# Kernel optimization log

Measured on AMD Instinct MI355X. Metric: run time of the kernel, lower is better.

The kernel has to match this reference:

```python
import jax, jax.numpy as jnp
import numpy as np

H = 1024
V = 50000
E_SOUND, E_NUM = 40, 5
D_SOUND, D_NUM = 32, 32
IN_DIM = H + D_SOUND + D_NUM  # GRU input size
B, L = 128, 128


def setup_inputs() -> dict:
    key = jax.random.key(0)
    ks = jax.random.split(key, 16)
    s = lambda k, shape: jax.random.normal(k, shape, jnp.float32) * 0.02
    return {
        "input_seq": jax.random.randint(ks[0], (B,), 0, V),
        "last_hidden": jax.random.normal(ks[1], (1, B, H), jnp.float32),
        "encoder_outputs": jax.random.normal(ks[2], (L, B, H), jnp.float32),
        "char2num": jax.random.randint(ks[3], (V,), 0, E_NUM),
        "char2final": jax.random.randint(ks[4], (V,), 0, E_SOUND),
        "emb": s(ks[5], (V, H)),
        "sound_emb": s(ks[6], (E_SOUND, D_SOUND)),
        "num_emb": s(ks[7], (E_NUM, D_NUM)),
        "W_ih": s(ks[8], (3 * H, IN_DIM)),
        "W_hh": s(ks[9], (3 * H, H)),
        "b_ih": jnp.zeros((3 * H,), jnp.float32),
        "b_hh": jnp.zeros((3 * H,), jnp.float32),
        "W_attn": s(ks[10], (H, H)),
        "b_attn": jnp.zeros((H,), jnp.float32),
        "W_cat": s(ks[11], (H, 2 * H)),
        "b_cat": jnp.zeros((H,), jnp.float32),
        "W_out": s(ks[12], (V, H)),
        "b_out": jnp.zeros((V,), jnp.float32),
    }


def _gru_cell(x, h, W_ih, W_hh, b_ih, b_hh):
    # PyTorch GRU gate order: r, z, n
    gi = x @ W_ih.T + b_ih
    gh = h @ W_hh.T + b_hh
    i_r, i_z, i_n = jnp.split(gi, 3, axis=-1)
    h_r, h_z, h_n = jnp.split(gh, 3, axis=-1)
    r = jax.nn.sigmoid(i_r + h_r)
    z = jax.nn.sigmoid(i_z + h_z)
    n = jnp.tanh(i_n + r * h_n)
    return (1.0 - z) * n + z * h


def reference(input_seq, last_hidden, encoder_outputs, char2num, char2final,
              emb, sound_emb, num_emb, W_ih, W_hh, b_ih, b_hh,
              W_attn, b_attn, W_cat, b_cat, W_out, b_out):
    # Embeddings (eval mode -> dropout is identity)
    e = emb[input_seq]                             # [B,H]
    num_ids = char2num[input_seq]                  # [B]
    snd_ids = char2final[input_seq]                # [B]
    x = jnp.concatenate([e, sound_emb[snd_ids], num_emb[num_ids]], -1)  # [B,IN_DIM]

    # Single-step single-layer GRU
    h_new = _gru_cell(x, last_hidden[0], W_ih, W_hh, b_ih, b_hh)  # [B,H]
    hidden = h_new[None]                            # [1,B,H]
    rnn_output = h_new                              # [B,H]

    # Luong 'general' attention, batched (replaces the nested-loop .mm calls)
    proj = jnp.einsum('lbh,kh->lbk', encoder_outputs, W_attn) + b_attn  # [L,B,H]
    energies = jnp.einsum('bh,lbh->bl', rnn_output, proj)               # [B,L]
    attn_weights = jax.nn.softmax(energies, axis=1)[:, None, :]         # [B,1,L]
    context = jnp.einsum('bl,lbh->bh', attn_weights[:, 0], encoder_outputs)

    concat_out = jnp.tanh(jnp.concatenate([rnn_output, context], -1) @ W_cat.T + b_cat)
    output = concat_out @ W_out.T + b_out           # [B,V]
    return output, hidden, attn_weights
```

## Files before the change

### kernel.cpp

```cpp
#include <hip/hip_runtime.h>
#include <hip/hip_bf16.h>
#include <cstddef>

#define B_   128
#define L_   128
#define H_   1024
#define V_   50000
#define INDIM 1088

typedef short short8 __attribute__((ext_vector_type(8)));
typedef unsigned short ushort8 __attribute__((ext_vector_type(8)));
typedef unsigned short ushort4v __attribute__((ext_vector_type(4)));
typedef float f32x4 __attribute__((ext_vector_type(4)));

static __device__ __forceinline__ unsigned short f2bf(float f) {
    unsigned u = __builtin_bit_cast(unsigned, f);
    u = u + 0x7FFFu + ((u >> 16) & 1u);
    return (unsigned short)(u >> 16);
}
static __device__ __forceinline__ float bf2f(unsigned short h) {
    unsigned u = ((unsigned)h) << 16;
    return __builtin_bit_cast(float, u);
}
static __device__ __forceinline__ float sigm(float v) {
    return 1.f / (1.f + __expf(-v));
}

__global__ __launch_bounds__(256) void prep_kernel(
    const int* __restrict__ seq, const int* __restrict__ c2n,
    const int* __restrict__ c2f, const float* __restrict__ emb,
    const float* __restrict__ semb, const float* __restrict__ nemb,
    const float* __restrict__ lh,
    unsigned short* __restrict__ x_hi, unsigned short* __restrict__ x_lo,
    unsigned short* __restrict__ h_hi, unsigned short* __restrict__ h_lo)
{
    const int b = blockIdx.x, t = threadIdx.x;
    const int idx = seq[b];
    for (int i = t; i < 528; i += 256) {
        float4 v;
        unsigned short *dh, *dl;
        int off;
        if (i < 272) {
            if (i < 256) {
                v = *(const float4*)&emb[(size_t)idx * H_ + i * 4];
            } else {
                const int j = i - 256;
                if (j < 8) v = *(const float4*)&semb[c2f[idx] * 32 + j * 4];
                else       v = *(const float4*)&nemb[c2n[idx] * 32 + (j - 8) * 4];
            }
            dh = x_hi + (size_t)b * INDIM; dl = x_lo + (size_t)b * INDIM; off = i * 4;
        } else {
            const int j = i - 272;
            v = *(const float4*)&lh[(size_t)b * H_ + j * 4];
            dh = h_hi + (size_t)b * H_; dl = h_lo + (size_t)b * H_; off = j * 4;
        }
        const float fv[4] = {v.x, v.y, v.z, v.w};
        ushort4v hh, ll;
#pragma unroll
        for (int e = 0; e < 4; e++) {
            hh[e] = f2bf(fv[e]);
            ll[e] = f2bf(fv[e] - bf2f(hh[e]));
        }
        *(ushort4v*)&dh[off] = hh;
        *(ushort4v*)&dl[off] = ll;
    }
}

template<bool WT, bool SPLIT, bool TANH>
static __device__ __forceinline__ void sgemm_body(
    const unsigned short* __restrict__ Ah, const unsigned short* __restrict__ Al, int lda,
    const float* __restrict__ W, int ldw,
    const float* __restrict__ bias,
    float* __restrict__ C, int ldc, size_t pstride,
    int N, int k_len0, int k_lenB)
{
    extern __shared__ char smem_raw[];
    typedef unsigned short RowT[72];
    RowT* As_h = (RowT*)(smem_raw);
    RowT* Ws_h = (RowT*)(smem_raw + 18432);
    RowT* As_l = (RowT*)(smem_raw + 27648);
    RowT* Ws_l = (RowT*)(smem_raw + 46080);

    const int t    = threadIdx.x;
    const int lane = t & 63;
    const int wv   = t >> 6;
    const int wr   = wv >> 1;
    const int wc   = wv & 1;
    const int n0   = blockIdx.x * 64;
    const int l15  = lane & 15;
    const int g    = lane >> 4;

    const int y     = blockIdx.y;
    const int k_off = (y == 0) ? 0 : k_len0 + (y - 1) * k_lenB;
    const int k_len = (y == 0) ? k_len0 : k_lenB;
    float* Cp = C + (size_t)y * pstride;

    const int ar = t >> 3;
    const int ac = (t & 7) * 8;
    const int wn = t >> 2, wq = t & 3;
    const int nk = t >> 4, nn4 = (t & 15) * 4;

    f32x4 acc[4][2];
#pragma unroll
    for (int i = 0; i < 4; i++)
#pragma unroll
        for (int j = 0; j < 2; j++) acc[i][j] = (f32x4){0.f, 0.f, 0.f, 0.f};

#define LOAD_A(K0, RA, RAL) do {                                               \
    _Pragma("unroll")                                                          \
    for (int i_ = 0; i_ < 4; i_++)                                             \
        RA[i_] = *(const ushort8*)&Ah[(size_t)(ar + i_ * 32) * lda + (K0) + ac]; \
    if constexpr (SPLIT) {                                                     \
        _Pragma("unroll")                                                      \
        for (int i_ = 0; i_ < 4; i_++)                                         \
            RAL[i_] = *(const ushort8*)&Al[(size_t)(ar + i_ * 32) * lda + (K0) + ac]; \
    }                                                                          \
} while (0)

#define LOAD_W(K0, RW) do {                                                    \
    if constexpr (WT) {                                                        \
        const bool ok_ = (n0 + wn) < N;                                        \
        const float* wb_ = W + (size_t)(n0 + wn) * ldw + (K0);                 \
        _Pragma("unroll")                                                      \
        for (int j_ = 0; j_ < 4; j_++)                                         \
            RW[j_] = ok_ ? *(const float4*)&wb_[j_ * 16 + wq * 4]              \
                         : make_float4(0.f, 0.f, 0.f, 0.f);                    \
    } else {                                                                   \
        _Pragma("unroll")                                                      \
        for (int j_ = 0; j_ < 4; j_++)                                         \
            RW[j_] = *(const float4*)&W[(size_t)((K0) + nk + j_ * 16) * ldw + n0 + nn4]; \
    }                                                                          \
} while (0)

#define STAGE_REGS(RA, RAL, RW) do {                                           \
    _Pragma("unroll")                                                          \
    for (int i_ = 0; i_ < 4; i_++) {                                           \
        *(ushort8*)&As_h[ar + i_ * 32][ac] = RA[i_];                           \
        if constexpr (SPLIT) *(ushort8*)&As_l[ar + i_ * 32][ac] = RAL[i_];     \
    }                                                                          \
    if constexpr (WT) {                                                        \
        _Pragma("unroll")                                                      \
        for (int j_ = 0; j_ < 4; j_++) {                                       \
            const float fv_[4] = {RW[j_].x, RW[j_].y, RW[j_].z, RW[j_].w};     \
            ushort4v hh_, ll_;                                                 \
            _Pragma("unroll")                                                  \
            for (int e_ = 0; e_ < 4; e_++) {                                   \
                hh_[e_] = f2bf(fv_[e_]);                                       \
                if constexpr (SPLIT) ll_[e_] = f2bf(fv_[e_] - bf2f(hh_[e_]));  \
            }                                                                  \
            *(ushort4v*)&Ws_h[wn][j_ * 16 + wq * 4] = hh_;                     \
            if constexpr (SPLIT) *(ushort4v*)&Ws_l[wn][j_ * 16 + wq * 4] = ll_; \
        }                                                                      \
    } else {                                                                   \
        _Pragma("unroll")                                                      \
        for (int j_ = 0; j_ < 4; j_++) {                                       \
            const float fv_[4] = {RW[j_].x, RW[j_].y, RW[j_].z, RW[j_].w};     \
            _Pragma("unroll")                                                  \
            for (int e_ = 0; e_ < 4; e_++) {                                   \
                const unsigned short hb_ = f2bf(fv_[e_]);                      \
                Ws_h[nn4 + e_][nk + j_ * 16] = hb_;                            \
                if constexpr (SPLIT)                                           \
                    Ws_l[nn4 + e_][nk + j_ * 16] = f2bf(fv_[e_] - bf2f(hb_));  \
            }                                                                  \
        }                                                                      \
    }                                                                          \
} while (0)

    const int k_end = k_off + k_len;

    ushort8 ra[4], ral[4], nra[4], nral[4];
    float4 rw0[4], rw1[4], rw2[4];

    LOAD_A(k_off, ra, ral);
    LOAD_W(k_off, rw0);
    if constexpr (!SPLIT) {
        if (k_off + 64 < k_end) LOAD_W(k_off + 64, rw1);
    }

    for (int k0 = k_off; k0 < k_end; k0 += 64) {
        const bool m1 = (k0 + 64) < k_end;
        const bool m2 = (k0 + 128) < k_end;
        if (m1) {
            LOAD_A(k0 + 64, nra, nral);
            if constexpr (SPLIT) LOAD_W(k0 + 64, rw1);
        }

        STAGE_REGS(ra, ral, rw0);
        __syncthreads();

        if constexpr (!SPLIT) {
            if (m2) LOAD_W(k0 + 128, rw2);
        }

#pragma unroll
        for (int ks = 0; ks < 2; ks++) {
            const int ko = ks * 32 + g * 8;
            short8 ah[4], bh[2];
#pragma unroll
            for (int mi = 0; mi < 4; mi++)
                ah[mi] = *(const short8*)&As_h[wr * 64 + mi * 16 + l15][ko];
#pragma unroll
            for (int ni = 0; ni < 2; ni++)
                bh[ni] = *(const short8*)&Ws_h[wc * 32 + ni * 16 + l15][ko];
            if constexpr (SPLIT) {
                short8 al[4], bl[2];
#pragma unroll
                for (int mi = 0; mi < 4; mi++)
                    al[mi] = *(const short8*)&As_l[wr * 64 + mi * 16 + l15][ko];
#pragma unroll
                for (int ni = 0; ni < 2; ni++)
                    bl[ni] = *(const short8*)&Ws_l[wc * 32 + ni * 16 + l15][ko];
#pragma unroll
                for (int mi = 0; mi < 4; mi++)
#pragma unroll
                    for (int ni = 0; ni < 2; ni++) {
                        acc[mi][ni] = __builtin_amdgcn_mfma_f32_16x16x32_bf16(ah[mi], bh[ni], acc[mi][ni], 0, 0, 0);
                        acc[mi][ni] = __builtin_amdgcn_mfma_f32_16x16x32_bf16(ah[mi], bl[ni], acc[mi][ni], 0, 0, 0);
                        acc[mi][ni] = __builtin_amdgcn_mfma_f32_16x16x32_bf16(al[mi], bh[ni], acc[mi][ni], 0, 0, 0);
                    }
            } else {
#pragma unroll
                for (int mi = 0; mi < 4; mi++)
#pragma unroll
                    for (int ni = 0; ni < 2; ni++)
                        acc[mi][ni] = __builtin_amdgcn_mfma_f32_16x16x32_bf16(ah[mi], bh[ni], acc[mi][ni], 0, 0, 0);
            }
        }
        __syncthreads();

        if (m1) {
#pragma unroll
            for (int i = 0; i < 4; i++) {
                ra[i] = nra[i];
                if constexpr (SPLIT) ral[i] = nral[i];
            }
#pragma unroll
            for (int j = 0; j < 4; j++) {
                rw0[j] = rw1[j];
                if constexpr (!SPLIT) rw1[j] = rw2[j];
            }
        }
    }
#undef LOAD_A
#undef LOAD_W
#undef STAGE_REGS

#pragma unroll
    for (int mi = 0; mi < 4; mi++) {
#pragma unroll
        for (int ni = 0; ni < 2; ni++) {
            const int col = n0 + wc * 32 + ni * 16 + l15;
            if (col < N) {
                const float bb = bias ? bias[col] : 0.f;
#pragma unroll
                for (int r = 0; r < 4; r++) {
                    const int row = wr * 64 + mi * 16 + g * 4 + r;
                    float v = acc[mi][ni][r] + bb;
                    if (TANH) v = tanhf(v);
                    Cp[(size_t)row * ldc + col] = v;
                }
            }
        }
    }
}

template<bool WT, bool SPLIT, bool TANH>
__global__ __launch_bounds__(256, 2) void sgemm(
    const unsigned short* __restrict__ Ah, const unsigned short* __restrict__ Al, int lda,
    const float* __restrict__ W, int ldw,
    const float* __restrict__ bias,
    float* __restrict__ C, int ldc, size_t pstride,
    int N, int k_len0, int k_lenB)
{
    sgemm_body<WT, SPLIT, TANH>(Ah, Al, lda, W, ldw, bias, C, ldc, pstride, N, k_len0, k_lenB);
}

__global__ __launch_bounds__(256, 2) void gru_gemm(
    const unsigned short* __restrict__ x_hi, const unsigned short* __restrict__ x_lo,
    const float* __restrict__ W_ih,
    const unsigned short* __restrict__ h_hi, const unsigned short* __restrict__ h_lo,
    const float* __restrict__ W_hh,
    float* __restrict__ gi, float* __restrict__ gh)
{
    if (blockIdx.z == 0)
        sgemm_body<true, true, false>(x_hi, x_lo, INDIM, W_ih, INDIM, nullptr,
                                      gi, 3072, (size_t)128 * 3072, 3072, 320, 256);
    else
        sgemm_body<true, true, false>(h_hi, h_lo, H_, W_hh, H_, nullptr,
                                      gh, 3072, (size_t)128 * 3072, 3072, 256, 256);
}

__global__ __launch_bounds__(256) void gru_gates_kernel(
    const float* __restrict__ gi, const float* __restrict__ gh,
    const float* __restrict__ b_ih, const float* __restrict__ b_hh,
    const float* __restrict__ h_prev,
    float* __restrict__ hid_out,
    unsigned short* __restrict__ cat_hi, unsigned short* __restrict__ cat_lo)
{
    const int id = blockIdx.x * 256 + threadIdx.x;
    const int b = id >> 10, j = id & 1023;
    const size_t base = (size_t)b * 3072 + j;
    float ir = b_ih[j], iz = b_ih[1024 + j], in_ = b_ih[2048 + j];
    float hr = b_hh[j], hz = b_hh[1024 + j], hn = b_hh[2048 + j];
#pragma unroll
    for (int p = 0; p < 4; p++) {
        const float* gp = gi + (size_t)p * (128 * 3072);
        const float* hp = gh + (size_t)p * (128 * 3072);
        ir += gp[base]; iz += gp[base + 1024]; in_ += gp[base + 2048];
        hr += hp[base]; hz += hp[base + 1024]; hn += hp[base + 2048];
    }
    const float r = sigm(ir + hr);
    const float z = sigm(iz + hz);
    const float n = tanhf(in_ + r * hn);
    const float h = (1.f - z) * n + z * h_prev[id];
    hid_out[id] = h;
    const unsigned short hb = f2bf(h);
    cat_hi[(size_t)b * 2048 + j] = hb;
    cat_lo[(size_t)b * 2048 + j] = f2bf(h - bf2f(hb));
}

__global__ __launch_bounds__(512) void energy_partial_kernel(
    const float* __restrict__ qp, const float* __restrict__ enc,
    float* __restrict__ epart)
{
    const int s = blockIdx.x, b = blockIdx.y;
    const int t = threadIdx.x, lane = t & 63, wv = t >> 6;
    __shared__ float q_s[256];
    if (t < 256) {
        const size_t o = (size_t)b * H_ + s * 256 + t;
        q_s[t] = qp[o] + qp[o + 131072] + qp[o + 262144] + qp[o + 393216];
    }
    __syncthreads();
    const float4 qv = *(const float4*)&q_s[lane * 4];
    const float* encb = enc + (size_t)b * H_ + s * 256;
    for (int l0 = 0; l0 < 16; l0++) {
        const int l = wv * 16 + l0;
        float4 ev = *(const float4*)&encb[(size_t)l * (B_ * H_) + lane * 4];
        float p = ev.x * qv.x + ev.y * qv.y + ev.z * qv.z + ev.w * qv.w;
#pragma unroll
        for (int off = 32; off > 0; off >>= 1) p += __shfl_xor(p, off);
        if (lane == 0) epart[((size_t)b * 128 + l) * 4 + s] = p;
    }
}

__global__ __launch_bounds__(256) void context_softmax_kernel(
    const float* __restrict__ epart, const float* __restrict__ enc,
    unsigned short* __restrict__ cat_hi, float* __restrict__ attnw)
{
    const int s = blockIdx.x, b = blockIdx.y, t = threadIdx.x;
    const int lane = t & 63, wv = t >> 6;
    __shared__ float w_s[128];
    __shared__ float red[4];

    float e = -INFINITY;
    if (t < 128) {
        float4 pe = *(const float4*)&epart[((size_t)b * 128 + t) * 4];
        e = pe.x + pe.y + pe.z + pe.w;
    }
    float mx = e;
#pragma unroll
    for (int off = 32; off > 0; off >>= 1) mx = fmaxf(mx, __shfl_xor(mx, off));
    if (lane == 0) red[wv] = mx;
    __syncthreads();
    const float gm = fmaxf(fmaxf(red[0], red[1]), fmaxf(red[2], red[3]));
    __syncthreads();
    float ex = (t < 128) ? __expf(e - gm) : 0.f;
    float sm = ex;
#pragma unroll
    for (int off = 32; off > 0; off >>= 1) sm += __shfl_xor(sm, off);
    if (lane == 0) red[wv] = sm;
    __syncthreads();
    const float gs = red[0] + red[1] + red[2] + red[3];
    if (t < 128) {
        const float w = ex / gs;
        w_s[t] = w;
        if (s == 0) attnw[(size_t)b * L_ + t] = w;
    }
    __syncthreads();

    const int h = s * 256 + t;
    const float* encb = enc + (size_t)b * H_ + h;
    float c = 0.f;
#pragma unroll 4
    for (int l = 0; l < 128; l++)
        c += w_s[l] * encb[(size_t)l * (B_ * H_)];
    cat_hi[(size_t)b * 2048 + 1024 + h] = f2bf(c);
}

__global__ __launch_bounds__(256) void co_reduce_kernel(
    const float* __restrict__ co_part, const float* __restrict__ b_cat,
    unsigned short* __restrict__ co_hi)
{
    const int id = blockIdx.x * 256 + threadIdx.x;
    const int j = id & 1023;
    float s = b_cat[j];
#pragma unroll
    for (int p = 0; p < 4; p++) s += co_part[(size_t)p * 131072 + id];
    co_hi[id] = f2bf(tanhf(s));
}

extern "C" void kernel_launch(void* const* d_in, const int* in_sizes, int n_in,
                              void* d_out, int out_size, void* d_ws, size_t ws_size,
                              hipStream_t stream)
{
    const int*   seq    = (const int*)  d_in[0];
    const float* lh     = (const float*)d_in[1];
    const float* enc    = (const float*)d_in[2];
    const int*   c2n    = (const int*)  d_in[3];
    const int*   c2f    = (const int*)  d_in[4];
    const float* emb    = (const float*)d_in[5];
    const float* semb   = (const float*)d_in[6];
    const float* nemb   = (const float*)d_in[7];
    const float* W_ih   = (const float*)d_in[8];
    const float* W_hh   = (const float*)d_in[9];
    const float* b_ih   = (const float*)d_in[10];
    const float* b_hh   = (const float*)d_in[11];
    const float* W_attn = (const float*)d_in[12];
    const float* W_cat  = (const float*)d_in[14];
    const float* b_cat  = (const float*)d_in[15];
    const float* W_out  = (const float*)d_in[16];
    const float* b_out  = (const float*)d_in[17];

    float* out    = (float*)d_out;
    float* hidden = out + (size_t)B_ * V_;
    float* attnw  = hidden + (size_t)B_ * H_;

    unsigned short* x_hi   = (unsigned short*)d_ws;
    unsigned short* x_lo   = x_hi   + (size_t)128 * INDIM;
    unsigned short* h_hi   = x_lo   + (size_t)128 * INDIM;
    unsigned short* h_lo   = h_hi   + (size_t)128 * 1024;
    unsigned short* cat_hi = h_lo   + (size_t)128 * 1024;
    unsigned short* cat_lo = cat_hi + (size_t)128 * 2048;
    unsigned short* co_hi  = cat_lo + (size_t)128 * 2048;
    float* fbase   = (float*)(co_hi + (size_t)128 * 1024);
    float* gi_part = fbase;
    float* gh_part = gi_part + (size_t)4 * 128 * 3072;
    float* q_part  = fbase;
    float* co_part = q_part + (size_t)4 * 128 * 1024;
    float* epart   = co_part + (size_t)4 * 128 * 1024;

    const int SMEM_SPLIT = 55296;
    const int SMEM_PLAIN = 27648;

    hipLaunchKernelGGL(prep_kernel, dim3(B_), dim3(256), 0, stream,
                       seq, c2n, c2f, emb, semb, nemb, lh, x_hi, x_lo, h_hi, h_lo);
    hipLaunchKernelGGL(gru_gemm, dim3(48, 4, 2), dim3(256), SMEM_SPLIT, stream,
                       x_hi, x_lo, W_ih, h_hi, h_lo, W_hh, gi_part, gh_part);
    hipLaunchKernelGGL(gru_gates_kernel, dim3(512), dim3(256), 0, stream,
                       gi_part, gh_part, b_ih, b_hh, lh, hidden, cat_hi, cat_lo);
    hipLaunchKernelGGL((sgemm<false, true, false>), dim3(16, 4), dim3(256), SMEM_SPLIT, stream,
                       cat_hi, cat_lo, 2048, W_attn, H_, (const float*)nullptr,
                       q_part, H_, (size_t)128 * 1024, H_, 256, 256);
    hipLaunchKernelGGL(energy_partial_kernel, dim3(4, 128), dim3(512), 0, stream,
                       q_part, enc, epart);
    hipLaunchKernelGGL(context_softmax_kernel, dim3(4, 128), dim3(256), 0, stream,
                       epart, enc, cat_hi, attnw);
    hipLaunchKernelGGL((sgemm<true, false, false>), dim3(16, 4), dim3(256), SMEM_PLAIN, stream,
                       cat_hi, cat_hi, 2048, W_cat, 2048, (const float*)nullptr,
                       co_part, H_, (size_t)128 * 1024, H_, 512, 512);
    hipLaunchKernelGGL(co_reduce_kernel, dim3(512), dim3(256), 0, stream,
                       co_part, b_cat, co_hi);
    hipLaunchKernelGGL((sgemm<true, false, false>), dim3((V_ + 63) / 64, 1), dim3(256), SMEM_PLAIN, stream,
                       co_hi, co_hi, H_, W_out, H_, b_out,
                       out, V_, (size_t)0, V_, H_, H_);
}
```

Measured before the change: 160.3 us.

## Replace LDS-tiled GEMMs with per-wave register GEMMs reading weights directly

Replaces the shared-memory tiled sgemm with wave-level GEMMs. Each wave owns 16 output columns across all 128 batch rows, loads its weight slice straight from global memory, converts it with packed bf16 conversion instructions, and feeds MFMA with A fragments read directly from global/L2. W_attn is pre-transposed and split into bf16 hi/lo inside the prep kernel so the attention-projection GEMM can read contiguous rows. This removes LDS staging and barriers and lets the weight stream flow without a block tile, but the A operand is reloaded from cache by every wave without LDS reuse. The hidden-state-independent transpose of W_attn is now redone on every call as extra work.

After: 302.8 us. 88.9% more time.

```diff
diff --git a/kernel.cpp b/kernel.cpp
--- a/kernel.cpp
+++ b/kernel.cpp
@@ -9,7 +9,6 @@
 #define INDIM 1088
 
 typedef short short8 __attribute__((ext_vector_type(8)));
-typedef unsigned short ushort8 __attribute__((ext_vector_type(8)));
 typedef unsigned short ushort4v __attribute__((ext_vector_type(4)));
 typedef float f32x4 __attribute__((ext_vector_type(4)));
 
@@ -26,268 +25,268 @@
     return 1.f / (1.f + __expf(-v));
 }
 
+static __device__ __forceinline__ unsigned cvt_pk(float lo, float hi) {
+    unsigned r;
+    asm("v_cvt_pk_bf16_f32 %0, %1, %2" : "=v"(r) : "v"(lo), "v"(hi));
+    return r;
+}
+static __device__ __forceinline__ short8 cvt8(float4 a, float4 b) {
+    union { unsigned u[4]; short8 s; } r;
+    r.u[0] = cvt_pk(a.x, a.y); r.u[1] = cvt_pk(a.z, a.w);
+    r.u[2] = cvt_pk(b.x, b.y); r.u[3] = cvt_pk(b.z, b.w);
+    return r.s;
+}
+static __device__ __forceinline__ void cvt8_split(float4 a, float4 b, short8& hi, short8& lo) {
+    const float f[8] = {a.x, a.y, a.z, a.w, b.x, b.y, b.z, b.w};
+    union { unsigned u[4]; short8 s; } rh, rl;
+#pragma unroll
+    for (int i = 0; i < 4; i++) {
+        const unsigned p = cvt_pk(f[2 * i], f[2 * i + 1]);
+        const float r0 = __builtin_bit_cast(float, p << 16);
+        const float r1 = __builtin_bit_cast(float, p & 0xFFFF0000u);
+        rh.u[i] = p;
+        rl.u[i] = cvt_pk(f[2 * i] - r0, f[2 * i + 1] - r1);
+    }
+    hi = rh.s; lo = rl.s;
+}
+
+#define MFMA(a, b, c) __builtin_amdgcn_mfma_f32_16x16x32_bf16((a), (b), (c), 0, 0, 0)
+
 __global__ __launch_bounds__(256) void prep_kernel(
     const int* __restrict__ seq, const int* __restrict__ c2n,
     const int* __restrict__ c2f, const float* __restrict__ emb,
     const float* __restrict__ semb, const float* __restrict__ nemb,
-    const float* __restrict__ lh,
+    const float* __restrict__ lh, const float* __restrict__ W_attn,
     unsigned short* __restrict__ x_hi, unsigned short* __restrict__ x_lo,
-    unsigned short* __restrict__ h_hi, unsigned short* __restrict__ h_lo)
-{
-    const int b = blockIdx.x, t = threadIdx.x;
-    const int idx = seq[b];
-    for (int i = t; i < 528; i += 256) {
-        float4 v;
-        unsigned short *dh, *dl;
-        int off;
-        if (i < 272) {
-            if (i < 256) {
-                v = *(const float4*)&emb[(size_t)idx * H_ + i * 4];
+    unsigned short* __restrict__ h_hi, unsigned short* __restrict__ h_lo,
+    unsigned short* __restrict__ wt_hi, unsigned short* __restrict__ wt_lo)
+{
+    __shared__ float tile[64][65];
+    const int t = threadIdx.x;
+    if (blockIdx.x < 128) {
+        const int b = blockIdx.x;
+        const int idx = seq[b];
+        for (int i = t; i < 528; i += 256) {
+            float4 v;
+            unsigned short *dh, *dl;
+            int off;
+            if (i < 272) {
+                if (i < 256) {
+                    v = *(const float4*)&emb[(size_t)idx * H_ + i * 4];
+                } else {
+                    const int j = i - 256;
+                    if (j < 8) v = *(const float4*)&semb[c2f[idx] * 32 + j * 4];
+                    else       v = *(const float4*)&nemb[c2n[idx] * 32 + (j - 8) * 4];
+                }
+                dh = x_hi + (size_t)b * INDIM; dl = x_lo + (size_t)b * INDIM; off = i * 4;
             } else {
-                const int j = i - 256;
-                if (j < 8) v = *(const float4*)&semb[c2f[idx] * 32 + j * 4];
-                else       v = *(const float4*)&nemb[c2n[idx] * 32 + (j - 8) * 4];
-            }
-            dh = x_hi + (size_t)b * INDIM; dl = x_lo + (size_t)b * INDIM; off = i * 4;
-        } else {
-            const int j = i - 272;
-            v = *(const float4*)&lh[(size_t)b * H_ + j * 4];
-            dh = h_hi + (size_t)b * H_; dl = h_lo + (size_t)b * H_; off = j * 4;
-        }
-        const float fv[4] = {v.x, v.y, v.z, v.w};
-        ushort4v hh, ll;
-#pragma unroll
-        for (int e = 0; e < 4; e++) {
-            hh[e] = f2bf(fv[e]);
-            ll[e] = f2bf(fv[e] - bf2f(hh[e]));
-        }
-        *(ushort4v*)&dh[off] = hh;
-        *(ushort4v*)&dl[off] = ll;
-    }
-}
-
-template<bool WT, bool SPLIT, bool TANH>
-static __device__ __forceinline__ void sgemm_body(
-    const unsigned short* __restrict__ Ah, const unsigned short* __restrict__ Al, int lda,
-    const float* __restrict__ W, int ldw,
-    const float* __restrict__ bias,
-    float* __restrict__ C, int ldc, size_t pstride,
-    int N, int k_len0, int k_lenB)
-{
-    extern __shared__ char smem_raw[];
-    typedef unsigned short RowT[72];
-    RowT* As_h = (RowT*)(smem_raw);
-    RowT* Ws_h = (RowT*)(smem_raw + 18432);
-    RowT* As_l = (RowT*)(smem_raw + 27648);
-    RowT* Ws_l = (RowT*)(smem_raw + 46080);
-
-    const int t    = threadIdx.x;
-    const int lane = t & 63;
-    const int wv   = t >> 6;
-    const int wr   = wv >> 1;
-    const int wc   = wv & 1;
-    const int n0   = blockIdx.x * 64;
-    const int l15  = lane & 15;
-    const int g    = lane >> 4;
-
-    const int y     = blockIdx.y;
-    const int k_off = (y == 0) ? 0 : k_len0 + (y - 1) * k_lenB;
-    const int k_len = (y == 0) ? k_len0 : k_lenB;
-    float* Cp = C + (size_t)y * pstride;
-
-    const int ar = t >> 3;
-    const int ac = (t & 7) * 8;
-    const int wn = t >> 2, wq = t & 3;
-    const int nk = t >> 4, nn4 = (t & 15) * 4;
-
-    f32x4 acc[4][2];
-#pragma unroll
-    for (int i = 0; i < 4; i++)
-#pragma unroll
-        for (int j = 0; j < 2; j++) acc[i][j] = (f32x4){0.f, 0.f, 0.f, 0.f};
-
-#define LOAD_A(K0, RA, RAL) do {                                               \
-    _Pragma("unroll")                                                          \
-    for (int i_ = 0; i_ < 4; i_++)                                             \
-        RA[i_] = *(const ushort8*)&Ah[(size_t)(ar + i_ * 32) * lda + (K0) + ac]; \
-    if constexpr (SPLIT) {                                                     \
-        _Pragma("unroll")                                                      \
-        for (int i_ = 0; i_ < 4; i_++)                                         \
-            RAL[i_] = *(const ushort8*)&Al[(size_t)(ar + i_ * 32) * lda + (K0) + ac]; \
-    }                                                                          \
-} while (0)
-
-#define LOAD_W(K0, RW) do {                                                    \
-    if constexpr (WT) {                                                        \
-        const bool ok_ = (n0 + wn) < N;                                        \
-        const float* wb_ = W + (size_t)(n0 + wn) * ldw + (K0);                 \
-        _Pragma("unroll")                                                      \
-        for (int j_ = 0; j_ < 4; j_++)                                         \
-            RW[j_] = ok_ ? *(const float4*)&wb_[j_ * 16 + wq * 4]              \
-                         : make_float4(0.f, 0.f, 0.f, 0.f);                    \
-    } else {                                                                   \
-        _Pragma("unroll")                                                      \
-        for (int j_ = 0; j_ < 4; j_++)                                         \
-            RW[j_] = *(const float4*)&W[(size_t)((K0) + nk + j_ * 16) * ldw + n0 + nn4]; \
-    }                                                                          \
-} while (0)
-
-#define STAGE_REGS(RA, RAL, RW) do {                                           \
-    _Pragma("unroll")                                                          \
-    for (int i_ = 0; i_ < 4; i_++) {                                           \
-        *(ushort8*)&As_h[ar + i_ * 32][ac] = RA[i_];                           \
-        if constexpr (SPLIT) *(ushort8*)&As_l[ar + i_ * 32][ac] = RAL[i_];     \
-    }                                                                          \
-    if constexpr (WT) {                                                        \
-        _Pragma("unroll")                                                      \
-        for (int j_ = 0; j_ < 4; j_++) {                                       \
-            const float fv_[4] = {RW[j_].x, RW[j_].y, RW[j_].z, RW[j_].w};     \
-            ushort4v hh_, ll_;                                                 \
-            _Pragma("unroll")                                                  \
-            for (int e_ = 0; e_ < 4; e_++) {                                   \
-                hh_[e_] = f2bf(fv_[e_]);                                       \
-                if constexpr (SPLIT) ll_[e_] = f2bf(fv_[e_] - bf2f(hh_[e_]));  \
-            }                                                                  \
-            *(ushort4v*)&Ws_h[wn][j_ * 16 + wq * 4] = hh_;                     \
-            if constexpr (SPLIT) *(ushort4v*)&Ws_l[wn][j_ * 16 + wq * 4] = ll_; \
-        }                                                                      \
-    } else {                                                                   \
-        _Pragma("unroll")                                                      \
-        for (int j_ = 0; j_ < 4; j_++) {                                       \
-            const float fv_[4] = {RW[j_].x, RW[j_].y, RW[j_].z, RW[j_].w};     \
-            _Pragma("unroll")                                                  \
-            for (int e_ = 0; e_ < 4; e_++) {                                   \
-                const unsigned short hb_ = f2bf(fv_[e_]);                      \
-                Ws_h[nn4 + e_][nk + j_ * 16] = hb_;                            \
-                if constexpr (SPLIT)                                           \
-                    Ws_l[nn4 + e_][nk + j_ * 16] = f2bf(fv_[e_] - bf2f(hb_));  \
-            }                                                                  \
-        }                                                                      \
-    }                                                                          \
-} while (0)
-
-    const int k_end = k_off + k_len;
-
-    ushort8 ra[4], ral[4], nra[4], nral[4];
-    float4 rw0[4], rw1[4], rw2[4];
-
-    LOAD_A(k_off, ra, ral);
-    LOAD_W(k_off, rw0);
-    if constexpr (!SPLIT) {
-        if (k_off + 64 < k_end) LOAD_W(k_off + 64, rw1);
-    }
-
-    for (int k0 = k_off; k0 < k_end; k0 += 64) {
-        const bool m1 = (k0 + 64) < k_end;
-        const bool m2 = (k0 + 128) < k_end;
-        if (m1) {
-            LOAD_A(k0 + 64, nra, nral);
-            if constexpr (SPLIT) LOAD_W(k0 + 64, rw1);
-        }
-
-        STAGE_REGS(ra, ral, rw0);
+                const int j = i - 272;
+                v = *(const float4*)&lh[(size_t)b * H_ + j * 4];
+                dh = h_hi + (size_t)b * H_; dl = h_lo + (size_t)b * H_; off = j * 4;
+            }
+            const float fv[4] = {v.x, v.y, v.z, v.w};
+            ushort4v hh, ll;
+#pragma unroll
+            for (int e = 0; e < 4; e++) {
+                hh[e] = f2bf(fv[e]);
+                ll[e] = f2bf(fv[e] - bf2f(hh[e]));
+            }
+            *(ushort4v*)&dh[off] = hh;
+            *(ushort4v*)&dl[off] = ll;
+        }
+    } else {
+        const int bid = blockIdx.x - 128;
+        const int n0 = (bid & 15) * 64, k0 = (bid >> 4) * 64;
+        const int c = t & 63, r4 = t >> 6;
+#pragma unroll
+        for (int i = 0; i < 16; i++) {
+            const int r = r4 * 16 + i;
+            tile[r][c] = W_attn[(size_t)(k0 + r) * H_ + n0 + c];
+        }
         __syncthreads();
-
-        if constexpr (!SPLIT) {
-            if (m2) LOAD_W(k0 + 128, rw2);
-        }
-
-#pragma unroll
-        for (int ks = 0; ks < 2; ks++) {
-            const int ko = ks * 32 + g * 8;
-            short8 ah[4], bh[2];
-#pragma unroll
-            for (int mi = 0; mi < 4; mi++)
-                ah[mi] = *(const short8*)&As_h[wr * 64 + mi * 16 + l15][ko];
-#pragma unroll
-            for (int ni = 0; ni < 2; ni++)
-                bh[ni] = *(const short8*)&Ws_h[wc * 32 + ni * 16 + l15][ko];
-            if constexpr (SPLIT) {
-                short8 al[4], bl[2];
-#pragma unroll
-                for (int mi = 0; mi < 4; mi++)
-                    al[mi] = *(const short8*)&As_l[wr * 64 + mi * 16 + l15][ko];
-#pragma unroll
-                for (int ni = 0; ni < 2; ni++)
-                    bl[ni] = *(const short8*)&Ws_l[wc * 32 + ni * 16 + l15][ko];
-#pragma unroll
-                for (int mi = 0; mi < 4; mi++)
-#pragma unroll
-                    for (int ni = 0; ni < 2; ni++) {
-                        acc[mi][ni] = __builtin_amdgcn_mfma_f32_16x16x32_bf16(ah[mi], bh[ni], acc[mi][ni], 0, 0, 0);
-                        acc[mi][ni] = __builtin_amdgcn_mfma_f32_16x16x32_bf16(ah[mi], bl[ni], acc[mi][ni], 0, 0, 0);
-                        acc[mi][ni] = __builtin_amdgcn_mfma_f32_16x16x32_bf16(al[mi], bh[ni], acc[mi][ni], 0, 0, 0);
-                    }
-            } else {
-#pragma unroll
-                for (int mi = 0; mi < 4; mi++)
-#pragma unroll
-                    for (int ni = 0; ni < 2; ni++)
-                        acc[mi][ni] = __builtin_amdgcn_mfma_f32_16x16x32_bf16(ah[mi], bh[ni], acc[mi][ni], 0, 0, 0);
-            }
-        }
-        __syncthreads();
-
-        if (m1) {
-#pragma unroll
-            for (int i = 0; i < 4; i++) {
-                ra[i] = nra[i];
-                if constexpr (SPLIT) ral[i] = nral[i];
-            }
-#pragma unroll
-            for (int j = 0; j < 4; j++) {
-                rw0[j] = rw1[j];
-                if constexpr (!SPLIT) rw1[j] = rw2[j];
-            }
-        }
-    }
-#undef LOAD_A
-#undef LOAD_W
-#undef STAGE_REGS
-
-#pragma unroll
-    for (int mi = 0; mi < 4; mi++) {
-#pragma unroll
-        for (int ni = 0; ni < 2; ni++) {
-            const int col = n0 + wc * 32 + ni * 16 + l15;
-            if (col < N) {
-                const float bb = bias ? bias[col] : 0.f;
-#pragma unroll
-                for (int r = 0; r < 4; r++) {
-                    const int row = wr * 64 + mi * 16 + g * 4 + r;
-                    float v = acc[mi][ni][r] + bb;
-                    if (TANH) v = tanhf(v);
-                    Cp[(size_t)row * ldc + col] = v;
-                }
-            }
-        }
-    }
-}
-
-template<bool WT, bool SPLIT, bool TANH>
-__global__ __launch_bounds__(256, 2) void sgemm(
-    const unsigned short* __restrict__ Ah, const unsigned short* __restrict__ Al, int lda,
-    const float* __restrict__ W, int ldw,
-    const float* __restrict__ bias,
-    float* __restrict__ C, int ldc, size_t pstride,
-    int N, int k_len0, int k_lenB)
-{
-    sgemm_body<WT, SPLIT, TANH>(Ah, Al, lda, W, ldw, bias, C, ldc, pstride, N, k_len0, k_lenB);
-}
-
-__global__ __launch_bounds__(256, 2) void gru_gemm(
+#pragma unroll
+        for (int i = 0; i < 16; i++) {
+            const int r = r4 * 16 + i;
+            const float f = tile[c][r];
+            const unsigned short hb = f2bf(f);
+            wt_hi[(size_t)(n0 + r) * H_ + k0 + c] = hb;
+            wt_lo[(size_t)(n0 + r) * H_ + k0 + c] = f2bf(f - bf2f(hb));
+        }
+    }
+}
+
+
+__global__ __launch_bounds__(256) void gru_wgemm(
     const unsigned short* __restrict__ x_hi, const unsigned short* __restrict__ x_lo,
     const float* __restrict__ W_ih,
     const unsigned short* __restrict__ h_hi, const unsigned short* __restrict__ h_lo,
     const float* __restrict__ W_hh,
     float* __restrict__ gi, float* __restrict__ gh)
 {
-    if (blockIdx.z == 0)
-        sgemm_body<true, true, false>(x_hi, x_lo, INDIM, W_ih, INDIM, nullptr,
-                                      gi, 3072, (size_t)128 * 3072, 3072, 320, 256);
-    else
-        sgemm_body<true, true, false>(h_hi, h_lo, H_, W_hh, H_, nullptr,
-                                      gh, 3072, (size_t)128 * 3072, 3072, 256, 256);
+    const int wid = blockIdx.x * 4 + (threadIdx.x >> 6);
+    const int lane = threadIdx.x & 63, l15 = lane & 15, g = lane >> 4;
+    const int y = wid & 3;
+    int tile = wid >> 2;
+    const unsigned short *Ah, *Al;
+    const float* W;
+    float* Cp;
+    int lda, K0, KL;
+    if (tile < 192) {
+        Ah = x_hi; Al = x_lo; W = W_ih; Cp = gi; lda = INDIM;
+        K0 = y ? 320 + (y - 1) * 256 : 0; KL = y ? 256 : 320;
+    } else {
+        tile -= 192;
+        Ah = h_hi; Al = h_lo; W = W_hh; Cp = gh; lda = H_;
+        K0 = y * 256; KL = 256;
+    }
+    const int n0 = tile * 16;
+    Cp += (size_t)y * (128 * 3072);
+    const float* Wb = W + (size_t)(n0 + l15) * lda;
+
+    f32x4 acc[8];
+#pragma unroll
+    for (int i = 0; i < 8; i++) acc[i] = (f32x4){0.f, 0.f, 0.f, 0.f};
+
+    for (int k0 = K0; k0 < K0 + KL; k0 += 64) {
+#pragma unroll
+        for (int ks = 0; ks < 2; ks++) {
+            const int k = k0 + ks * 32 + g * 8;
+            const float4 w0 = *(const float4*)&Wb[k];
+            const float4 w1 = *(const float4*)&Wb[k + 4];
+            short8 bh, bl;
+            cvt8_split(w0, w1, bh, bl);
+#pragma unroll
+            for (int mi = 0; mi < 8; mi++) {
+                const short8 ah = *(const short8*)&Ah[(size_t)(mi * 16 + l15) * lda + k];
+                const short8 al = *(const short8*)&Al[(size_t)(mi * 16 + l15) * lda + k];
+                acc[mi] = MFMA(ah, bh, acc[mi]);
+                acc[mi] = MFMA(ah, bl, acc[mi]);
+                acc[mi] = MFMA(al, bh, acc[mi]);
+            }
+        }
+    }
+    const int col = n0 + l15;
+#pragma unroll
+    for (int mi = 0; mi < 8; mi++)
+#pragma unroll
+        for (int r = 0; r < 4; r++)
+            Cp[(size_t)(mi * 16 + g * 4 + r) * 3072 + col] = acc[mi][r];
+}
+
+__global__ __launch_bounds__(256) void q_wgemm(
+    const unsigned short* __restrict__ cat_hi, const unsigned short* __restrict__ cat_lo,
+    const unsigned short* __restrict__ wt_hi, const unsigned short* __restrict__ wt_lo,
+    float* __restrict__ q_part)
+{
+    const int wid = blockIdx.x * 4 + (threadIdx.x >> 6);
+    const int lane = threadIdx.x & 63, l15 = lane & 15, g = lane >> 4;
+    const int y = wid & 3, tile = wid >> 2;
+    const int n0 = tile * 16, K0 = y * 256;
+    float* Cp = q_part + (size_t)y * (128 * 1024);
+    const unsigned short* Bh = wt_hi + (size_t)(n0 + l15) * H_;
+    const unsigned short* Bl = wt_lo + (size_t)(n0 + l15) * H_;
+
+    f32x4 acc[8];
+#pragma unroll
+    for (int i = 0; i < 8; i++) acc[i] = (f32x4){0.f, 0.f, 0.f, 0.f};
+
+    for (int k0 = K0; k0 < K0 + 256; k0 += 64) {
+#pragma unroll
+        for (int ks = 0; ks < 2; ks++) {
+            const int k = k0 + ks * 32 + g * 8;
+            const short8 bh = *(const short8*)&Bh[k];
+            const short8 bl = *(const short8*)&Bl[k];
+#pragma unroll
+            for (int mi = 0; mi < 8; mi++) {
+                const short8 ah = *(const short8*)&cat_hi[(size_t)(mi * 16 + l15) * 2048 + k];
+                const short8 al = *(const short8*)&cat_lo[(size_t)(mi * 16 + l15) * 2048 + k];
+                acc[mi] = MFMA(ah, bh, acc[mi]);
+                acc[mi] = MFMA(ah, bl, acc[mi]);
+                acc[mi] = MFMA(al, bh, acc[mi]);
+            }
+        }
+    }
+    const int col = n0 + l15;
+#pragma unroll
+    for (int mi = 0; mi < 8; mi++)
+#pragma unroll
+        for (int r = 0; r < 4; r++)
+            Cp[(size_t)(mi * 16 + g * 4 + r) * 1024 + col] = acc[mi][r];
+}
+
+__global__ __launch_bounds__(256) void cat_wgemm(
+    const unsigned short* __restrict__ cat_hi, const float* __restrict__ W_cat,
+    float* __restrict__ co_part)
+{
+    const int wid = blockIdx.x * 4 + (threadIdx.x >> 6);
+    const int lane = threadIdx.x & 63, l15 = lane & 15, g = lane >> 6 ? 0 : lane >> 4;
+    const int gg = (threadIdx.x & 63) >> 4;
+    const int y = wid & 3, tile = wid >> 2;
+    const int n0 = tile * 16, K0 = y * 512;
+    float* Cp = co_part + (size_t)y * (128 * 1024);
+    const float* Wb = W_cat + (size_t)(n0 + l15) * 2048;
+
+    f32x4 acc[8];
+#pragma unroll
+    for (int i = 0; i < 8; i++) acc[i] = (f32x4){0.f, 0.f, 0.f, 0.f};
+
+    for (int k0 = K0; k0 < K0 + 512; k0 += 64) {
+#pragma unroll
+        for (int ks = 0; ks < 2; ks++) {
+            const int k = k0 + ks * 32 + gg * 8;
+            const float4 w0 = *(const float4*)&Wb[k];
+            const float4 w1 = *(const float4*)&Wb[k + 4];
+            const short8 bh = cvt8(w0, w1);
+#pragma unroll
+            for (int mi = 0; mi < 8; mi++) {
+                const short8 ah = *(const short8*)&cat_hi[(size_t)(mi * 16 + l15) * 2048 + k];
+                acc[mi] = MFMA(ah, bh, acc[mi]);
+            }
+        }
+    }
+    const int col = n0 + l15;
+#pragma unroll
+    for (int mi = 0; mi < 8; mi++)
+#pragma unroll
+        for (int r = 0; r < 4; r++)
+            Cp[(size_t)(mi * 16 + gg * 4 + r) * 1024 + col] = acc[mi][r];
+}
+
+__global__ __launch_bounds__(256) void out_wgemm(
+    const unsigned short* __restrict__ co_hi, const float* __restrict__ W_out,
+    const float* __restrict__ b_out, float* __restrict__ C)
+{
+    const int wid = blockIdx.x * 4 + (threadIdx.x >> 6);
+    if (wid >= 3125) return;
+    const int lane = threadIdx.x & 63, l15 = lane & 15, g = lane >> 4;
+    const int n0 = wid * 16;
+    const float* Wb = W_out + (size_t)(n0 + l15) * H_;
+
+    f32x4 acc[8];
+#pragma unroll
+    for (int i = 0; i < 8; i++) acc[i] = (f32x4){0.f, 0.f, 0.f, 0.f};
+
+    for (int k0 = 0; k0 < 1024; k0 += 64) {
+#pragma unroll
+        for (int ks = 0; ks < 2; ks++) {
+            const int k = k0 + ks * 32 + g * 8;
+            const float4 w0 = *(const float4*)&Wb[k];
+            const float4 w1 = *(const float4*)&Wb[k + 4];
+            const short8 bh = cvt8(w0, w1);
+#pragma unroll
+            for (int mi = 0; mi < 8; mi++) {
+                const short8 ah = *(const short8*)&co_hi[(size_t)(mi * 16 + l15) * 1024 + k];
+                acc[mi] = MFMA(ah, bh, acc[mi]);
+            }
+        }
+    }
+    const int col = n0 + l15;
+    const float bb = b_out[col];
+#pragma unroll
+    for (int mi = 0; mi < 8; mi++)
+#pragma unroll
+        for (int r = 0; r < 4; r++)
+            C[(size_t)(mi * 16 + g * 4 + r) * V_ + col] = acc[mi][r] + bb;
 }
 
 __global__ __launch_bounds__(256) void gru_gates_kernel(
@@ -432,35 +431,32 @@
     unsigned short* cat_hi = h_lo   + (size_t)128 * 1024;
     unsigned short* cat_lo = cat_hi + (size_t)128 * 2048;
     unsigned short* co_hi  = cat_lo + (size_t)128 * 2048;
-    float* fbase   = (float*)(co_hi + (size_t)128 * 1024);
+    unsigned short* wt_hi  = co_hi  + (size_t)128 * 1024;
+    unsigned short* wt_lo  = wt_hi  + (size_t)1024 * 1024;
+    float* fbase   = (float*)(wt_lo + (size_t)1024 * 1024);
     float* gi_part = fbase;
     float* gh_part = gi_part + (size_t)4 * 128 * 3072;
     float* q_part  = fbase;
     float* co_part = q_part + (size_t)4 * 128 * 1024;
     float* epart   = co_part + (size_t)4 * 128 * 1024;
 
-    const int SMEM_SPLIT = 55296;
-    const int SMEM_PLAIN = 27648;
-
-    hipLaunchKernelGGL(prep_kernel, dim3(B_), dim3(256), 0, stream,
-                       seq, c2n, c2f, emb, semb, nemb, lh, x_hi, x_lo, h_hi, h_lo);
-    hipLaunchKernelGGL(gru_gemm, dim3(48, 4, 2), dim3(256), SMEM_SPLIT, stream,
+    hipLaunchKernelGGL(prep_kernel, dim3(128 + 256), dim3(256), 0, stream,
+                       seq, c2n, c2f, emb, semb, nemb, lh, W_attn,
+                       x_hi, x_lo, h_hi, h_lo, wt_hi, wt_lo);
+    hipLaunchKernelGGL(gru_wgemm, dim3(384), dim3(256), 0, stream,
                        x_hi, x_lo, W_ih, h_hi, h_lo, W_hh, gi_part, gh_part);
     hipLaunchKernelGGL(gru_gates_kernel, dim3(512), dim3(256), 0, stream,
                        gi_part, gh_part, b_ih, b_hh, lh, hidden, cat_hi, cat_lo);
-    hipLaunchKernelGGL((sgemm<false, true, false>), dim3(16, 4), dim3(256), SMEM_SPLIT, stream,
-                       cat_hi, cat_lo, 2048, W_attn, H_, (const float*)nullptr,
-                       q_part, H_, (size_t)128 * 1024, H_, 256, 256);
+    hipLaunchKernelGGL(q_wgemm, dim3(64), dim3(256), 0, stream,
+                       cat_hi, cat_lo, wt_hi, wt_lo, q_part);
     hipLaunchKernelGGL(energy_partial_kernel, dim3(4, 128), dim3(512), 0, stream,
                        q_part, enc, epart);
     hipLaunchKernelGGL(context_softmax_kernel, dim3(4, 128), dim3(256), 0, stream,
                        epart, enc, cat_hi, attnw);
-    hipLaunchKernelGGL((sgemm<true, false, false>), dim3(16, 4), dim3(256), SMEM_PLAIN, stream,
-                       cat_hi, cat_hi, 2048, W_cat, 2048, (const float*)nullptr,
-                       co_part, H_, (size_t)128 * 1024, H_, 512, 512);
+    hipLaunchKernelGGL(cat_wgemm, dim3(64), dim3(256), 0, stream,
+                       cat_hi, W_cat, co_part);
     hipLaunchKernelGGL(co_reduce_kernel, dim3(512), dim3(256), 0, stream,
                        co_part, b_cat, co_hi);
-    hipLaunchKernelGGL((sgemm<true, false, false>), dim3((V_ + 63) / 64, 1), dim3(256), SMEM_PLAIN, stream,
-                       co_hi, co_hi, H_, W_out, H_, b_out,
-                       out, V_, (size_t)0, V_, H_, H_);
-}
+    hipLaunchKernelGGL(out_wgemm, dim3(782), dim3(256), 0, stream,
+                       co_hi, W_out, b_out, out);
+}
```

## Replace output projection GEMM with direct-to-LDS double-buffered fp32 weight streaming kernel

Applied to the files above, without the earlier changes.

Adds a dedicated kernel for the vocabulary projection. It streams W_out rows from global memory straight into swizzled LDS using global_load_lds, double-buffered with explicit vmcnt waits. Weights are converted to bf16 in registers with packed cvt instructions, and the activation fragments are read directly from global memory. The aim is to overlap the large weight stream with MFMA work and cut register staging and conversion overhead, at the cost of hand-tuned waitcnt/barrier synchronisation and repeated uncached-LDS reads of the A operand.

New measurement: 178.6 us. 1.11x slower.

```diff
diff --git a/kernel.cpp b/kernel.cpp
--- a/kernel.cpp
+++ b/kernel.cpp
@@ -25,6 +25,26 @@
 static __device__ __forceinline__ float sigm(float v) {
     return 1.f / (1.f + __expf(-v));
 }
+
+static __device__ __forceinline__ unsigned cvt_pk(float lo, float hi) {
+    unsigned r;
+    asm("v_cvt_pk_bf16_f32 %0, %1, %2" : "=v"(r) : "v"(lo), "v"(hi));
+    return r;
+}
+static __device__ __forceinline__ short8 cvt8(float4 a, float4 b) {
+    union { unsigned u[4]; short8 s; } r;
+    r.u[0] = cvt_pk(a.x, a.y); r.u[1] = cvt_pk(a.z, a.w);
+    r.u[2] = cvt_pk(b.x, b.y); r.u[3] = cvt_pk(b.z, b.w);
+    return r.s;
+}
+
+static __device__ __forceinline__ void gload16(const float* g, float* l) {
+    __builtin_amdgcn_global_load_lds(
+        (const __attribute__((address_space(1))) unsigned*)g,
+        (__attribute__((address_space(3))) unsigned*)l, 16, 0, 0);
+}
+
+#define MFMA(a, b, c) __builtin_amdgcn_mfma_f32_16x16x32_bf16((a), (b), (c), 0, 0, 0)
 
 __global__ __launch_bounds__(256) void prep_kernel(
     const int* __restrict__ seq, const int* __restrict__ c2n,
@@ -214,16 +234,16 @@
                 for (int mi = 0; mi < 4; mi++)
 #pragma unroll
                     for (int ni = 0; ni < 2; ni++) {
-                        acc[mi][ni] = __builtin_amdgcn_mfma_f32_16x16x32_bf16(ah[mi], bh[ni], acc[mi][ni], 0, 0, 0);
-                        acc[mi][ni] = __builtin_amdgcn_mfma_f32_16x16x32_bf16(ah[mi], bl[ni], acc[mi][ni], 0, 0, 0);
-                        acc[mi][ni] = __builtin_amdgcn_mfma_f32_16x16x32_bf16(al[mi], bh[ni], acc[mi][ni], 0, 0, 0);
+                        acc[mi][ni] = MFMA(ah[mi], bh[ni], acc[mi][ni]);
+                        acc[mi][ni] = MFMA(ah[mi], bl[ni], acc[mi][ni]);
+                        acc[mi][ni] = MFMA(al[mi], bh[ni], acc[mi][ni]);
                     }
             } else {
 #pragma unroll
                 for (int mi = 0; mi < 4; mi++)
 #pragma unroll
                     for (int ni = 0; ni < 2; ni++)
-                        acc[mi][ni] = __builtin_amdgcn_mfma_f32_16x16x32_bf16(ah[mi], bh[ni], acc[mi][ni], 0, 0, 0);
+                        acc[mi][ni] = MFMA(ah[mi], bh[ni], acc[mi][ni]);
             }
         }
         __syncthreads();
@@ -288,6 +308,102 @@
     else
         sgemm_body<true, true, false>(h_hi, h_lo, H_, W_hh, H_, nullptr,
                                       gh, 3072, (size_t)128 * 3072, 3072, 256, 256);
+}
+
+__global__ __launch_bounds__(256, 4) void out_gemm2(
+    const unsigned short* __restrict__ co_hi,
+    const float* __restrict__ W_out,
+    const float* __restrict__ b_out,
+    float* __restrict__ C)
+{
+    __shared__ float buf[2][4096];
+    const int t = threadIdx.x;
+    const int lane = t & 63;
+    const int wv = t >> 6;
+    const int wr = wv >> 1, wc = wv & 1;
+    const int l15 = lane & 15, g = lane >> 4;
+    const int n0 = blockIdx.x * 64;
+
+    const float* rowp[4];
+    int colo[4];
+#pragma unroll
+    for (int r = 0; r < 4; r++) {
+        const int s = r * 256 + t;
+        const int row = s >> 4;
+        const int col4 = (s & 15) ^ (row & 7);
+        const int grow = min(n0 + row, V_ - 1);
+        rowp[r] = W_out + (size_t)grow * H_;
+        colo[r] = col4 * 4;
+    }
+
+#define OSTAGE(CUR, K0) do {                                                  \
+    _Pragma("unroll")                                                         \
+    for (int r_ = 0; r_ < 4; r_++)                                            \
+        gload16(rowp[r_] + (K0) + colo[r_], &buf[CUR][r_ * 1024 + t * 4]);    \
+} while (0)
+
+#define OLRD(CUR, ROW, C4) (*(const float4*)((const char*)(&buf[CUR][0]) +    \
+    ((ROW) * 256 + ((((C4) ^ ((ROW) & 7))) << 4))))
+
+    f32x4 acc[4][2];
+#pragma unroll
+    for (int i = 0; i < 4; i++)
+#pragma unroll
+        for (int j = 0; j < 2; j++) acc[i][j] = (f32x4){0.f, 0.f, 0.f, 0.f};
+
+    OSTAGE(0, 0);
+    OSTAGE(1, 64);
+
+    for (int it = 0; it < 16; ++it) {
+        const int cur = it & 1;
+        const int k0 = it * 64;
+        if (it < 15) asm volatile("s_waitcnt vmcnt(4)" ::: "memory");
+        else         asm volatile("s_waitcnt vmcnt(0)" ::: "memory");
+        __builtin_amdgcn_s_barrier();
+
+#pragma unroll
+        for (int ks = 0; ks < 2; ks++) {
+            const int k = k0 + ks * 32 + g * 8;
+            const int c4 = ks * 8 + g * 2;
+            short8 bh[2];
+#pragma unroll
+            for (int ni = 0; ni < 2; ni++) {
+                const int row = wc * 32 + ni * 16 + l15;
+                float4 w0 = cur ? OLRD(1, row, c4)     : OLRD(0, row, c4);
+                float4 w1 = cur ? OLRD(1, row, c4 + 1) : OLRD(0, row, c4 + 1);
+                bh[ni] = cvt8(w0, w1);
+            }
+#pragma unroll
+            for (int mi = 0; mi < 4; mi++) {
+                const short8 ah = *(const short8*)&co_hi[(size_t)(wr * 64 + mi * 16 + l15) * H_ + k];
+#pragma unroll
+                for (int ni = 0; ni < 2; ni++)
+                    acc[mi][ni] = MFMA(ah, bh[ni], acc[mi][ni]);
+            }
+        }
+        asm volatile("s_waitcnt lgkmcnt(0)" ::: "memory");
+        __builtin_amdgcn_sched_barrier(0);
+        __builtin_amdgcn_s_barrier();
+        if (it + 2 < 16) {
+            if (cur) OSTAGE(1, k0 + 128);
+            else     OSTAGE(0, k0 + 128);
+        }
+    }
+#undef OSTAGE
+#undef OLRD
+
+#pragma unroll
+    for (int mi = 0; mi < 4; mi++)
+#pragma unroll
+        for (int ni = 0; ni < 2; ni++) {
+            const int col = n0 + wc * 32 + ni * 16 + l15;
+            if (col < V_) {
+                const float bb = b_out[col];
+#pragma unroll
+                for (int r = 0; r < 4; r++)
+                    C[(size_t)(wr * 64 + mi * 16 + g * 4 + r) * V_ + col] = acc[mi][ni][r] + bb;
+            }
+        }
 }
 
 __global__ __launch_bounds__(256) void gru_gates_kernel(
@@ -460,7 +576,6 @@
                        co_part, H_, (size_t)128 * 1024, H_, 512, 512);
     hipLaunchKernelGGL(co_reduce_kernel, dim3(512), dim3(256), 0, stream,
                        co_part, b_cat, co_hi);
-    hipLaunchKernelGGL((sgemm<true, false, false>), dim3((V_ + 63) / 64, 1), dim3(256), SMEM_PLAIN, stream,
-                       co_hi, co_hi, H_, W_out, H_, b_out,
-                       out, V_, (size_t)0, V_, H_, H_);
-}
+    hipLaunchKernelGGL(out_gemm2, dim3((V_ + 63) / 64), dim3(256), 0, stream,
+                       co_hi, W_out, b_out, out);
+}
```

## Drop split-bf16 in GRU GEMMs and fuse hidden-half W_cat GEMM with attention query

Applied to the files above, without the earlier changes.

The GRU input/hidden GEMMs switch from hi+lo split bf16 operands to plain bf16, halving the MFMA work and shared memory for that stage. The attention-query GEMM is merged into one launch with the first half of the W_cat GEMM (the rnn_output part, which doesn't depend on context), leaving only the context half after the softmax. This removes GEMM work from the critical path after attention and cuts one launch. The cost is reduced accuracy in the GRU gates, since the low bf16 residual of activations is no longer used.

Measured after the change: 154.8 us (median of 2 runs). 3.5% less time.

```diff
diff --git a/kernel.cpp b/kernel.cpp
--- a/kernel.cpp
+++ b/kernel.cpp
@@ -276,18 +276,33 @@
 }
 
 __global__ __launch_bounds__(256, 2) void gru_gemm(
-    const unsigned short* __restrict__ x_hi, const unsigned short* __restrict__ x_lo,
+    const unsigned short* __restrict__ x_hi,
     const float* __restrict__ W_ih,
-    const unsigned short* __restrict__ h_hi, const unsigned short* __restrict__ h_lo,
+    const unsigned short* __restrict__ h_hi,
     const float* __restrict__ W_hh,
     float* __restrict__ gi, float* __restrict__ gh)
 {
     if (blockIdx.z == 0)
-        sgemm_body<true, true, false>(x_hi, x_lo, INDIM, W_ih, INDIM, nullptr,
-                                      gi, 3072, (size_t)128 * 3072, 3072, 320, 256);
+        sgemm_body<true, false, false>(x_hi, x_hi, INDIM, W_ih, INDIM, nullptr,
+                                       gi, 3072, (size_t)128 * 3072, 3072, 320, 256);
     else
-        sgemm_body<true, true, false>(h_hi, h_lo, H_, W_hh, H_, nullptr,
-                                      gh, 3072, (size_t)128 * 3072, 3072, 256, 256);
+        sgemm_body<true, false, false>(h_hi, h_hi, H_, W_hh, H_, nullptr,
+                                       gh, 3072, (size_t)128 * 3072, 3072, 256, 256);
+}
+
+__global__ __launch_bounds__(256, 2) void q_cat_kernel(
+    const unsigned short* __restrict__ cat_hi, const unsigned short* __restrict__ cat_lo,
+    const float* __restrict__ W_attn, const float* __restrict__ W_cat,
+    float* __restrict__ q_part, float* __restrict__ co_part)
+{
+    if (blockIdx.z == 0) {
+        sgemm_body<false, true, false>(cat_hi, cat_lo, 2048, W_attn, H_, nullptr,
+                                       q_part, H_, (size_t)128 * 1024, H_, 256, 256);
+    } else {
+        if (blockIdx.y >= 2) return;
+        sgemm_body<true, false, false>(cat_hi, cat_hi, 2048, W_cat, 2048, nullptr,
+                                       co_part, H_, (size_t)128 * 1024, H_, 512, 512);
+    }
 }
 
 __global__ __launch_bounds__(256) void gru_gates_kernel(
@@ -444,20 +459,21 @@
 
     hipLaunchKernelGGL(prep_kernel, dim3(B_), dim3(256), 0, stream,
                        seq, c2n, c2f, emb, semb, nemb, lh, x_hi, x_lo, h_hi, h_lo);
-    hipLaunchKernelGGL(gru_gemm, dim3(48, 4, 2), dim3(256), SMEM_SPLIT, stream,
-                       x_hi, x_lo, W_ih, h_hi, h_lo, W_hh, gi_part, gh_part);
+    hipLaunchKernelGGL(gru_gemm, dim3(48, 4, 2), dim3(256), SMEM_PLAIN, stream,
+                       x_hi, W_ih, h_hi, W_hh, gi_part, gh_part);
     hipLaunchKernelGGL(gru_gates_kernel, dim3(512), dim3(256), 0, stream,
                        gi_part, gh_part, b_ih, b_hh, lh, hidden, cat_hi, cat_lo);
-    hipLaunchKernelGGL((sgemm<false, true, false>), dim3(16, 4), dim3(256), SMEM_SPLIT, stream,
-                       cat_hi, cat_lo, 2048, W_attn, H_, (const float*)nullptr,
-                       q_part, H_, (size_t)128 * 1024, H_, 256, 256);
+    hipLaunchKernelGGL(q_cat_kernel, dim3(16, 4, 2), dim3(256), SMEM_SPLIT, stream,
+                       cat_hi, cat_lo, W_attn, W_cat, q_part, co_part);
     hipLaunchKernelGGL(energy_partial_kernel, dim3(4, 128), dim3(512), 0, stream,
                        q_part, enc, epart);
     hipLaunchKernelGGL(context_softmax_kernel, dim3(4, 128), dim3(256), 0, stream,
                        epart, enc, cat_hi, attnw);
-    hipLaunchKernelGGL((sgemm<true, false, false>), dim3(16, 4), dim3(256), SMEM_PLAIN, stream,
-                       cat_hi, cat_hi, 2048, W_cat, 2048, (const float*)nullptr,
-                       co_part, H_, (size_t)128 * 1024, H_, 512, 512);
+    hipLaunchKernelGGL((sgemm<true, false, false>), dim3(16, 2), dim3(256), SMEM_PLAIN, stream,
+                       cat_hi + 1024, cat_hi + 1024, 2048, W_cat + 1024, 2048,
+                       (const float*)nullptr,
+                       co_part + (size_t)2 * 128 * 1024, H_, (size_t)128 * 1024,
+                       H_, 512, 512);
     hipLaunchKernelGGL(co_reduce_kernel, dim3(512), dim3(256), 0, stream,
                        co_part, b_cat, co_hi);
     hipLaunchKernelGGL((sgemm<true, false, false>), dim3((V_ + 63) / 64, 1), dim3(256), SMEM_PLAIN, stream,
```
